# Kernel tuning notes

Hardware: AMD Instinct MI355X
Metric: run time of the kernel (lower is better)

The kernel has to match this reference:

```python
import jax, jax.numpy as jnp
import numpy as np

N, E, P = 50000, 800000, 100000
IN, HID, K = 128, 128, 2


def _tagconv(h, nw, src, dst, n, W, b, k=K):
    # DGL TAGConv with edge_weight: k edge-weighted SpMM hops, concat, linear.
    feats = [h]
    for _ in range(k):
        m = feats[-1][src] * nw[:, None]          # [E, d] gather-multiply
        feats.append(jax.ops.segment_sum(m, dst, num_segments=n))
    return jnp.concatenate(feats, axis=-1) @ W.T + b


def setup_inputs() -> dict:
    key = jax.random.key(0)
    ks = jax.random.split(key, 24)
    inp = {
        "x": jax.random.normal(ks[0], (N, IN), jnp.float32),
        "w": jax.random.uniform(ks[1], (E,), jnp.float32, 0.01, 1.0),
        "src": jax.random.randint(ks[2], (E,), 0, N),
        "dst": jax.random.randint(ks[3], (E,), 0, N),
        "pos_src": jax.random.randint(ks[4], (P,), 0, N),
        "pos_dst": jax.random.randint(ks[5], (P,), 0, N),
        "neg_src": jax.random.randint(ks[6], (P,), 0, N),
        "neg_dst": jax.random.randint(ks[7], (P,), 0, N),
        # TAGConv linear weights: [hid, (k+1)*d_in]
        "W0": jax.random.normal(ks[8], (HID, (K + 1) * IN), jnp.float32) * 0.05,
        "b0": jnp.zeros((HID,), jnp.float32),
        "W1": jax.random.normal(ks[9], (HID, (K + 1) * HID), jnp.float32) * 0.05,
        "b1": jnp.zeros((HID,), jnp.float32),
        "W2": jax.random.normal(ks[10], (HID, (K + 1) * HID), jnp.float32) * 0.05,
        "b2": jnp.zeros((HID,), jnp.float32),
        # predictor MLP
        "Wp1": jax.random.normal(ks[11], (HID, HID), jnp.float32) * 0.05,
        "bp1": jnp.zeros((HID,), jnp.float32),
        "Wp2": jax.random.normal(ks[12], (HID, HID), jnp.float32) * 0.05,
        "bp2": jnp.zeros((HID,), jnp.float32),
        "Wp3": jax.random.normal(ks[13], (1, HID), jnp.float32) * 0.05,
        "bp3": jnp.zeros((1,), jnp.float32),
    }
    return inp


def reference(x, w, src, dst, pos_src, pos_dst, neg_src, neg_dst,
              W0, b0, W1, b1, W2, b2, Wp1, bp1, Wp2, bp2, Wp3, bp3):
    n = x.shape[0]
    # EdgeWeightNorm('both'): w_e / sqrt(deg_out_w(src) * deg_in_w(dst))
    deg_out = jax.ops.segment_sum(w, src, num_segments=n)
    deg_in = jax.ops.segment_sum(w, dst, num_segments=n)
    denom = jnp.sqrt(jnp.clip(deg_out[src] * deg_in[dst], 1e-12))
    nw = w / denom

    h = _tagconv(x, nw, src, dst, n, W0, b0)
    h = jax.nn.relu(h)
    h = _tagconv(h, nw, src, dst, n, W1, b1)
    h = jax.nn.relu(h)
    h = _tagconv(h, nw, src, dst, n, W2, b2)

    def predictor(z):
        z = jax.nn.relu(z @ Wp1.T + bp1)
        z = jax.nn.relu(z @ Wp2.T + bp2)
        return z @ Wp3.T + bp3

    h_pos = predictor(h[pos_src] * h[pos_dst])
    h_neg = predictor(h[neg_src] * h[neg_dst])
    return h_pos, h_neg, h
```

## Files before the change

### kernel.cpp

```cpp
#include <hip/hip_runtime.h>
#include <stdint.h>


#define D128 128

typedef __bf16 v8bf __attribute__((ext_vector_type(8)));
typedef float v4f __attribute__((ext_vector_type(4)));
typedef uint32_t v4u __attribute__((ext_vector_type(4)));
typedef unsigned short ushort_t;

union BFU { v4u u; v8bf b; uint4 q; };

__device__ __forceinline__ uint32_t pack_hl(float f) {
  uint32_t hi = __float_as_uint(f) & 0xffff0000u;
  float lo = f - __uint_as_float(hi);
  return hi | (__float_as_uint(lo) >> 16);
}
__device__ __forceinline__ float unpack_hl(uint32_t p) {
  return __uint_as_float(p & 0xffff0000u) + __uint_as_float(p << 16);
}
__device__ __forceinline__ uint32_t f2bf_rn(float f) {
  uint32_t u = __float_as_uint(f);
  return (u + 0x7fffu + ((u >> 16) & 1u)) >> 16;
}
// ... 130 lines not shown
#pragma unroll
    for (int k = 0; k < 4; ++k) { uint32_t tmp = ws4[k]; ws4[k] = a; a += tmp; }
  }
  __syncthreads();
  uint32_t ex = x - v + ws4[wid];
  cur[t] = ex;
  int d = hb * 256 + t;
  if (d < N) rowptr[d] = b + (int)ex;
  __syncthreads();
  for (int i = b + t; i < e; i += 256) {
    uint2 el = bufD[i];
    uint32_t lo = (el.x >> 16) & 255u;
    uint32_t pos = atomicAdd(&cur[lo], 1u);
    esw[b + pos] = make_uint2(el.x & 0xffffu, el.y);
  }
}

__global__ void k_sub_src(const uint2* __restrict__ bufS,
                          const uint32_t* __restrict__ baseS,
                          float* __restrict__ deg_out, int N) {
  __shared__ float acc[256];
  int hb = blockIdx.x, t = threadIdx.x;
  acc[t] = 0.f;
  __syncthreads();
  int b = (int)baseS[hb], e = (int)baseS[hb + 1];
  for (int i = b + t; i < e; i += 256)
    atomicAdd(&acc[bufS[i].x & 255u], __uint_as_float(bufS[i].y));
  __syncthreads();
  int s = hb * 256 + t;
  if (s < N) deg_out[s] = acc[t];
}

__global__ void k_norm(const float* __restrict__ deg_out, const int* __restrict__ rowptr,
                       uint2* __restrict__ esw, int n) {
  int row = blockIdx.x * 4 + (threadIdx.x >> 6);
  if (row >= n) return;
  int lane = threadIdx.x & 63;
  int b0 = rowptr[row];
  int cnt = rowptr[row + 1] - b0;
  if (cnt <= 64) {
    uint32_t key = 0xffffffffu;
    float val = 0.f;
    if (lane < cnt) {
      uint2 e = esw[b0 + lane];
      key = e.x;
      val = __uint_as_float(e.y);
    }
    float s = val;
#pragma unroll
    for (int d = 32; d; d >>= 1) s += __shfl_xor(s, d);
#pragma unroll
    for (int k = 2; k <= 64; k <<= 1) {
#pragma unroll
      for (int j = k >> 1; j > 0; j >>= 1) {
        uint32_t ok = (uint32_t)__shfl_xor((int)key, j);
        float ov = __shfl_xor(val, j);
        bool asc = ((lane & k) == 0);
        bool lower = ((lane & j) == 0);
        bool take_min = (lower == asc);
        bool sw = take_min ? (ok < key) : (ok > key);
        if (sw) { key = ok; val = ov; }
      }
    }
    if (lane < cnt) {
      float dout = deg_out[key];
      float nw = val / sqrtf(fmaxf(dout * s, 1e-12f));
      esw[b0 + lane] = make_uint2(key, __float_as_uint(nw));
    }
  } else {
    float s = 0.f;
    for (int i = lane; i < cnt; i += 64) s += __uint_as_float(esw[b0 + i].y);
#pragma unroll
    for (int d = 32; d; d >>= 1) s += __shfl_xor(s, d);
    for (int i = lane; i < cnt; i += 64) {
      uint2 e = esw[b0 + i];
      float dout = deg_out[e.x];
      float nw = __uint_as_float(e.y) / sqrtf(fmaxf(dout * s, 1e-12f));
      esw[b0 + i] = make_uint2(e.x, __float_as_uint(nw));
    }
  }
}


__global__ void k_pack4(const float* __restrict__ in, uint32_t* __restrict__ Xp,
                        uint32_t* __restrict__ Xb, int n4) {
  int i = blockIdx.x * 256 + threadIdx.x;
  if (i >= n4) return;
  float4 f = ((const float4*)in)[i];
  ((uint4*)Xp)[i] = make_uint4(pack_hl(f.x), pack_hl(f.y), pack_hl(f.z), pack_hl(f.w));
  uint2 b;
  b.x = f2bf_rn(f.x) | (f2bf_rn(f.y) << 16);
  b.y = f2bf_rn(f.z) | (f2bf_rn(f.w) << 16);
  ((uint2*)Xb)[i] = b;
}

__global__ void k_packW(const float* __restrict__ p0, const float* __restrict__ p1,
                        const float* __restrict__ p2, const float* __restrict__ p3,
                        const float* __restrict__ p4, ushort_t* __restrict__ out) {
  int i = blockIdx.x * 256 + threadIdx.x;
  if (i >= 180224) return;
  float f;
  if (i < 49152) f = p0[i];
  else if (i < 98304) f = p1[i - 49152];
  else if (i < 147456) f = p2[i - 98304];
  else if (i < 163840) f = p3[i - 147456];
  else f = p4[i - 163840];
  out[i] = (ushort_t)f2bf_rn(f);
}


__global__ void k_spmm(const uint32_t* __restrict__ X, uint32_t* __restrict__ Y,
                       const uint2* __restrict__ esw, const int* __restrict__ rowptr,
                       int n) {
  int row = blockIdx.x * 4 + (threadIdx.x >> 6);
  if (row >= n) return;
  int lane = threadIdx.x & 63;
  int b0 = rowptr[row];
  int cnt = rowptr[row + 1] - b0;
  const uint32_t* __restrict__ Xl = X + lane;
  float a0 = 0.f, a1 = 0.f, c0 = 0.f, c1 = 0.f;
  for (int cbase = 0; cbase < cnt; cbase += 64) {
    int cc = min(64, cnt - cbase);
    int srcv = 0, wbits = 0;
    if (lane < cc) {
      uint2 e = esw[(size_t)b0 + cbase + lane];
      srcv = (int)e.x;
      wbits = (int)e.y;
    }
    int i = 0;
    for (; i + 8 <= cc; i += 8) {
      uint32_t u[8];
      float wv[8];
#pragma unroll
      for (int j = 0; j < 8; ++j) {
        int sj = __builtin_amdgcn_readlane(srcv, i + j);
        wv[j] = __uint_as_float(__builtin_amdgcn_readlane(wbits, i + j));
        u[j] = Xl[(size_t)sj * 64];
      }
#pragma unroll
      for (int j = 0; j < 8; j += 2) {
        a0 = fmaf(wv[j], bflo(u[j]), a0);
        a1 = fmaf(wv[j], bfhi(u[j]), a1);
        c0 = fmaf(wv[j + 1], bflo(u[j + 1]), c0);
        c1 = fmaf(wv[j + 1], bfhi(u[j + 1]), c1);
      }
    }
    for (; i < cc; ++i) {
      int sj = __builtin_amdgcn_readlane(srcv, i);
      float w0 = __uint_as_float(__builtin_amdgcn_readlane(wbits, i));
      uint32_t u0 = Xl[(size_t)sj * 64];
      a0 = fmaf(w0, bflo(u0), a0);
      a1 = fmaf(w0, bfhi(u0), a1);
    }
  }
  Y[(size_t)row * 64 + lane] = f2bf_rn(a0 + c0) | (f2bf_rn(a1 + c1) << 16);
}


__device__ __forceinline__ void build_frags(const uint32_t* __restrict__ p,
                                            v8bf& hi, v8bf& lo) {
  uint4 q0 = *(const uint4*)p;
  uint4 q1 = *(const uint4*)(p + 4);
  BFU uh, ul;
  uh.u[0] = (q0.x >> 16) | (q0.y & 0xffff0000u);
  uh.u[1] = (q0.z >> 16) | (q0.w & 0xffff0000u);
  uh.u[2] = (q1.x >> 16) | (q1.y & 0xffff0000u);
  uh.u[3] = (q1.z >> 16) | (q1.w & 0xffff0000u);
  ul.u[0] = (q0.x & 0xffffu) | (q0.y << 16);
  ul.u[1] = (q0.z & 0xffffu) | (q0.w << 16);
  ul.u[2] = (q1.x & 0xffffu) | (q1.y << 16);
  ul.u[3] = (q1.z & 0xffffu) | (q1.w << 16);
  hi = uh.b;
  lo = ul.b;
}

__global__ __launch_bounds__(256) void k_gemm(
    const uint32_t* __restrict__ F0hl, const uint32_t* __restrict__ F1b,
    const uint32_t* __restrict__ F2b, const ushort_t* __restrict__ Wb,
    const float* __restrict__ bias, int relu, int M,
    uint32_t* __restrict__ outp, ushort_t* __restrict__ outh,
    float* __restrict__ outf) {
  __shared__ ushort_t Wl[128 * 128];
  const int t = threadIdx.x;
  const int lane = t & 63;
  const int wave = t >> 6;
  const int wr = wave >> 1, wc = wave & 1;
  const int row0 = blockIdx.x * 64;
  const int l15 = lane & 15;
  const int kg = lane >> 4;

  int arow[2];
#pragma unroll
  for (int mr = 0; mr < 2; ++mr)
    arow[mr] = min(row0 + wr * 32 + mr * 16 + l15, M - 1);
  int wcol[4];
  float bv[4];
#pragma unroll
  for (int nr = 0; nr < 4; ++nr) {
    wcol[nr] = wc * 64 + nr * 16 + l15;
    bv[nr] = bias[wcol[nr]];
  }

  v4f acc[2][4];
#pragma unroll
  for (int mr = 0; mr < 2; ++mr)
#pragma unroll
    for (int nr = 0; nr < 4; ++nr) acc[mr][nr] = (v4f){0.f, 0.f, 0.f, 0.f};

  const int sc = t >> 1;
  const int sh = t & 1;

  for (int seg = 0; seg < 3; ++seg) {
    __syncthreads();
    {
      const ushort_t* gp = Wb + (size_t)sc * 384 + seg * 128 + sh * 64;
#pragma unroll
      for (int gi = 0; gi < 8; ++gi) {
        int gg = sh * 8 + gi;
        uint4 v = *(const uint4*)(gp + gi * 8);
        *(uint4*)((char*)Wl + sc * 256 + ((gg ^ (sc & 7)) * 16)) = v;
      }
    }
    __syncthreads();
    for (int kc = 0; kc < 128; kc += 32) {
      const int ko = kc + kg * 8;
      if (seg == 0) {
        v8bf ah[2], al[2];
#pragma unroll
        for (int mr = 0; mr < 2; ++mr)
          build_frags(F0hl + (size_t)arow[mr] * D128 + ko, ah[mr], al[mr]);
#pragma unroll
        for (int nr = 0; nr < 4; ++nr) {
          int col = wcol[nr];
          int g = (kc >> 3) + kg;
          v8bf bf = *(const v8bf*)((const char*)Wl + col * 256 + ((g ^ (col & 7)) * 16));
#pragma unroll
          for (int mr = 0; mr < 2; ++mr) {
            acc[mr][nr] = __builtin_amdgcn_mfma_f32_16x16x32_bf16(ah[mr], bf, acc[mr][nr], 0, 0, 0);
            acc[mr][nr] = __builtin_amdgcn_mfma_f32_16x16x32_bf16(al[mr], bf, acc[mr][nr], 0, 0, 0);
          }
        }
      } else {
        const uint32_t* __restrict__ Fb = (seg == 1) ? F1b : F2b;
        v8bf af[2];
#pragma unroll
        for (int mr = 0; mr < 2; ++mr) {
          BFU u;
          u.q = *(const uint4*)(Fb + (size_t)arow[mr] * 64 + (kc >> 1) + kg * 4);
          af[mr] = u.b;
        }
#pragma unroll
        for (int nr = 0; nr < 4; ++nr) {
          int col = wcol[nr];
          int g = (kc >> 3) + kg;
          v8bf bf = *(const v8bf*)((const char*)Wl + col * 256 + ((g ^ (col & 7)) * 16));
#pragma unroll
          for (int mr = 0; mr < 2; ++mr)
            acc[mr][nr] = __builtin_amdgcn_mfma_f32_16x16x32_bf16(af[mr], bf, acc[mr][nr], 0, 0, 0);
        }
      }
    }
  }

  __syncthreads();

#pragma unroll
  for (int mr = 0; mr < 2; ++mr) {
#pragma unroll
    for (int nr = 0; nr < 4; ++nr) {
      v4f a = acc[mr][nr];
#pragma unroll
      for (int r = 0; r < 4; ++r) {
        int row = row0 + wr * 32 + mr * 16 + kg * 4 + r;
        if (row < M) {
          float v = a[r] + bv[nr];
          if (relu) v = fmaxf(v, 0.f);
          size_t o = (size_t)row * D128 + wcol[nr];
          if (outp) outp[o] = pack_hl(v);
          if (outh) outh[o] = (ushort_t)f2bf_rn(v);
          if (outf) outf[o] = v;
        }
      }
    }
  }
}


__global__ __launch_bounds__(256) void k_pred(
    const uint32_t* __restrict__ Hb, const int* __restrict__ pos_src,
    const int* __restrict__ pos_dst, const int* __restrict__ neg_src,
    const int* __restrict__ neg_dst, const ushort_t* __restrict__ W1,
    const ushort_t* __restrict__ W2, const float* __restrict__ b1,
    const float* __restrict__ b2, const float* __restrict__ w3,
    const float* __restrict__ b3, int P, float* __restrict__ out) {
  __shared__ ushort_t Wl[128 * 128];
  const int t = threadIdx.x;
  const int lane = t & 63;
  const int wave = t >> 6;
  const int l15 = lane & 15;
  const int kg = lane >> 4;
  const int q = blockIdx.x * 64 + wave * 16 + l15;
  const int P2 = 2 * P;
  const bool valid = q < P2;
  const int qc = valid ? q : (P2 - 1);
  const int ia = (qc < P) ? pos_src[qc] : neg_src[qc - P];
  const int ib = (qc < P) ? pos_dst[qc] : neg_dst[qc - P];

  const int sc = t >> 1;
  const int sh = t & 1;

  {
    const ushort_t* gp = W1 + sc * 128 + sh * 64;
#pragma unroll
    for (int gi = 0; gi < 8; ++gi) {
      int gg = sh * 8 + gi;
      uint4 v = *(const uint4*)(gp + gi * 8);
      *(uint4*)((char*)Wl + sc * 256 + ((gg ^ (sc & 7)) * 16)) = v;
    }
  }

  v8bf zf[4];
#pragma unroll
  for (int kc = 0; kc < 4; ++kc) {
    uint4 qa = *(const uint4*)(Hb + (size_t)ia * 64 + kc * 16 + kg * 4);
    uint4 qb = *(const uint4*)(Hb + (size_t)ib * 64 + kc * 16 + kg * 4);
    BFU z;
    z.u[0] = bfmul2(qa.x, qb.x);
    z.u[1] = bfmul2(qa.y, qb.y);
    z.u[2] = bfmul2(qa.z, qb.z);
    z.u[3] = bfmul2(qa.w, qb.w);
    zf[kc] = z.b;
  }
  __syncthreads();

  v4f acc1[8];
#pragma unroll
  for (int nr = 0; nr < 8; ++nr) acc1[nr] = (v4f){0.f, 0.f, 0.f, 0.f};
#pragma unroll
  for (int kc = 0; kc < 4; ++kc) {
#pragma unroll
    for (int nr = 0; nr < 8; ++nr) {
      int c = nr * 16 + l15;
      int g = 4 * kc + kg;
      v8bf wf = *(const v8bf*)((const char*)Wl + c * 256 + ((g ^ (c & 7)) * 16));
      acc1[nr] = __builtin_amdgcn_mfma_f32_16x16x32_bf16(wf, zf[kc], acc1[nr], 0, 0, 0);
    }
  }

  uint32_t pk[8][2];
#pragma unroll
  for (int nr = 0; nr < 8; ++nr) {
    float v[4];
#pragma unroll
    for (int r = 0; r < 4; ++r) {
      int c = nr * 16 + kg * 4 + r;
      v[r] = fmaxf(acc1[nr][r] + b1[c], 0.f);
    }
    pk[nr][0] = f2bf_rn(v[0]) | (f2bf_rn(v[1]) << 16);
    pk[nr][1] = f2bf_rn(v[2]) | (f2bf_rn(v[3]) << 16);
  }

  __syncthreads();
  {
    const ushort_t* gp = W2 + sc * 128 + sh * 64;
#pragma unroll
    for (int gi = 0; gi < 8; ++gi) {
      int gg = sh * 8 + gi;
      uint4 v = *(const uint4*)(gp + gi * 8);
      *(uint4*)((char*)Wl + sc * 256 + ((gg ^ (sc & 7)) * 16)) = v;
    }
  }
  __syncthreads();

  v4f acc2[8];
#pragma unroll
  for (int nr = 0; nr < 8; ++nr) acc2[nr] = (v4f){0.f, 0.f, 0.f, 0.f};
#pragma unroll
  for (int kc = 0; kc < 4; ++kc) {
    BFU y;
#pragma unroll
    for (int d = 0; d < 4; ++d) {
      int srcLane = l15 + 16 * ((kg & 1) * 2 + (d >> 1));
      int va = __shfl((int)pk[2 * kc][d & 1], srcLane);
      int vb = __shfl((int)pk[2 * kc + 1][d & 1], srcLane);
      y.u[d] = (kg & 2) ? (uint32_t)vb : (uint32_t)va;
    }
#pragma unroll
    for (int nr = 0; nr < 8; ++nr) {
      int c = nr * 16 + l15;
      int g = 4 * kc + kg;
      v8bf wf = *(const v8bf*)((const char*)Wl + c * 256 + ((g ^ (c & 7)) * 16));
      acc2[nr] = __builtin_amdgcn_mfma_f32_16x16x32_bf16(wf, y.b, acc2[nr], 0, 0, 0);
    }
  }

  float s = 0.f;
#pragma unroll
  for (int nr = 0; nr < 8; ++nr) {
#pragma unroll
    for (int r = 0; r < 4; ++r) {
      int c = nr * 16 + kg * 4 + r;
      s += fmaxf(acc2[nr][r] + b2[c], 0.f) * w3[c];
    }
  }
  s += __shfl_xor(s, 16);
  s += __shfl_xor(s, 32);
  if (valid && kg == 0) out[q] = s + b3[0];
}


extern "C" void kernel_launch(void* const* d_in, const int* in_sizes, int n_in,
                              void* d_out, int out_size, void* d_ws, size_t ws_size,
                              hipStream_t stream) {
  const float* x = (const float*)d_in[0];
  const float* w = (const float*)d_in[1];
  const int* src = (const int*)d_in[2];
  const int* dst = (const int*)d_in[3];
  const int* pos_src = (const int*)d_in[4];
  const int* pos_dst = (const int*)d_in[5];
  const int* neg_src = (const int*)d_in[6];
  const int* neg_dst = (const int*)d_in[7];
  const float* W0 = (const float*)d_in[8];
  const float* b0 = (const float*)d_in[9];
  const float* W1 = (const float*)d_in[10];
  const float* b1 = (const float*)d_in[11];
  const float* W2 = (const float*)d_in[12];
  const float* b2 = (const float*)d_in[13];
  const float* Wp1 = (const float*)d_in[14];
  const float* bp1 = (const float*)d_in[15];
  const float* Wp2 = (const float*)d_in[16];
  const float* bp2 = (const float*)d_in[17];
  const float* Wp3 = (const float*)d_in[18];
  const float* bp3 = (const float*)d_in[19];

  const int N = in_sizes[0] / D128;
  const int E = in_sizes[1];
  const int P = in_sizes[4];

  float* out = (float*)d_out;
  float* h_fin = out + 2 * (size_t)P;
  uint32_t* Hp = (uint32_t*)h_fin;

  char* p = (char*)d_ws;
#define WALLOC(T, name, bytes) \
  T name = (T)p;               \
  p += (((size_t)(bytes) + 255) & ~(size_t)255);
  WALLOC(uint32_t*, meta, (size_t)(4 * 256 + 2 * 257) * 4)
  WALLOC(float*, deg_out, (size_t)N * 4)
  WALLOC(int*, rowptr, (size_t)(N + 1) * 4)
  WALLOC(uint2*, bufD, (size_t)E * 8)
  WALLOC(uint2*, bufS, (size_t)E * 8)
  WALLOC(uint2*, esw, (size_t)E * 8)
  WALLOC(ushort_t*, Wpk, (size_t)180224 * 2)
  WALLOC(uint32_t*, Xp, (size_t)N * D128 * 4)
  WALLOC(uint32_t*, Xb, (size_t)N * 64 * 4)
  WALLOC(uint32_t*, A, (size_t)N * 64 * 4)
  WALLOC(uint32_t*, B, (size_t)N * 64 * 4)
  WALLOC(uint32_t*, Hbuf, (size_t)N * 64 * 4)
#undef WALLOC

  uint32_t* histD = meta;
  uint32_t* histS = meta + 256;
  uint32_t* curD = meta + 512;
  uint32_t* curS = meta + 768;
  uint32_t* baseD = meta + 1024;
  uint32_t* baseS = meta + 1024 + 257;

  const ushort_t* W0b = Wpk;
  const ushort_t* W1b = Wpk + 49152;
  const ushort_t* W2b = Wpk + 98304;
  const ushort_t* Wp1b = Wpk + 147456;
  const ushort_t* Wp2b = Wpk + 163840;

  const int rb = (N + 3) / 4;
  const int gg = (N + 63) / 64;
  const int nHi = (N + 255) >> 8;

  hipMemsetAsync(meta, 0, 4 * 256 * 4, stream);
  k_hist2<<<128, 256, 0, stream>>>(src, dst, E, histD, histS);
  k_scan2<<<1, 256, 0, stream>>>(histD, histS, curD, baseD, curS, baseS, rowptr, N, E);
  k_part_dst<<<128, 256, 0, stream>>>(src, dst, w, E, curD, bufD);
  k_part_src<<<128, 256, 0, stream>>>(src, w, E, curS, bufS);
  k_sub_dst<<<nHi, 256, 0, stream>>>(bufD, baseD, esw, rowptr, N);
  k_sub_src<<<nHi, 256, 0, stream>>>(bufS, baseS, deg_out, N);
  k_norm<<<rb, 256, 0, stream>>>(deg_out, rowptr, esw, N);

  k_pack4<<<(N * 32 + 255) / 256, 256, 0, stream>>>(x, Xp, Xb, N * 32);
  k_packW<<<(180224 + 255) / 256, 256, 0, stream>>>(W0, W1, W2, Wp1, Wp2, Wpk);

  k_spmm<<<rb, 256, 0, stream>>>(Xb, A, esw, rowptr, N);
  k_spmm<<<rb, 256, 0, stream>>>(A, B, esw, rowptr, N);
  k_gemm<<<gg, 256, 0, stream>>>(Xp, A, B, W0b, b0, 1, N, Hp, (ushort_t*)Hbuf, nullptr);
  k_spmm<<<rb, 256, 0, stream>>>(Hbuf, A, esw, rowptr, N);
  k_spmm<<<rb, 256, 0, stream>>>(A, B, esw, rowptr, N);
  k_gemm<<<gg, 256, 0, stream>>>(Hp, A, B, W1b, b1, 1, N, Xp, (ushort_t*)Hbuf, nullptr);
  k_spmm<<<rb, 256, 0, stream>>>(Hbuf, A, esw, rowptr, N);
  k_spmm<<<rb, 256, 0, stream>>>(A, B, esw, rowptr, N);
  k_gemm<<<gg, 256, 0, stream>>>(Xp, A, B, W2b, b2, 0, N, nullptr, (ushort_t*)B, h_fin);

  k_pred<<<(2 * P + 63) / 64, 256, 0, stream>>>(B, pos_src, pos_dst, neg_src, neg_dst,
                                                Wp1b, Wp2b, bp1, bp2, Wp3, bp3, P, out);
}
```

Before: 454.0 us.

## Half-wave SpMM rows, prefetched GEMM operands, and src-sorted predictor queries

The SpMM now assigns two rows per wave, each 32-lane half loading 8 bytes per neighbor, which halves the wave count and widens loads. The GEMM prefetches A-operand fragments into registers before the weight-staging barrier so global latency overlaps LDS staging. Predictor queries are bucket-sorted by source node through three new small kernels, so gathered rows have better cache locality. The cost is extra launches and register pressure, plus divergence when the two rows in a wave have very different degrees.

```diff
diff --git a/kernel.cpp b/kernel.cpp
--- a/kernel.cpp
+++ b/kernel.cpp
@@ -236,6 +236,71 @@
 }
 
 
+__global__ void k_phist(const int* __restrict__ pos_src, const int* __restrict__ neg_src,
+                        int P, uint32_t* __restrict__ ph) {
+  __shared__ uint32_t h[256];
+  int t = threadIdx.x;
+  h[t] = 0;
+  __syncthreads();
+  int P2 = 2 * P;
+  for (int iq = blockIdx.x * 256 + t; iq < P2; iq += gridDim.x * 256) {
+    int ia = (iq < P) ? pos_src[iq] : neg_src[iq - P];
+    atomicAdd(&h[((unsigned)ia) >> 8], 1u);
+  }
+  __syncthreads();
+  if (h[t]) atomicAdd(&ph[t], h[t]);
+}
+
+__global__ void k_pscan(const uint32_t* __restrict__ ph, uint32_t* __restrict__ pcur) {
+  __shared__ uint32_t ws4[4];
+  int t = threadIdx.x;
+  int lane = t & 63, wid = t >> 6;
+  uint32_t v = ph[t], x = v;
+#pragma unroll
+  for (int d = 1; d < 64; d <<= 1) {
+    uint32_t y = (uint32_t)__shfl_up((int)x, d);
+    if (lane >= d) x += y;
+  }
+  if (lane == 63) ws4[wid] = x;
+  __syncthreads();
+  if (t == 0) {
+    uint32_t a = 0;
+#pragma unroll
+    for (int k = 0; k < 4; ++k) { uint32_t tmp = ws4[k]; ws4[k] = a; a += tmp; }
+  }
+  __syncthreads();
+  pcur[t] = x - v + ws4[wid];
+}
+
+__global__ void k_ppart(const int* __restrict__ pos_src, const int* __restrict__ neg_src,
+                        int P, uint32_t* __restrict__ pcur,
+                        uint32_t* __restrict__ qsorted) {
+  __shared__ uint32_t lh[256], lbase[256];
+  int t = threadIdx.x;
+  int P2 = 2 * P;
+  int per = (P2 + gridDim.x - 1) / gridDim.x;
+  int e0 = blockIdx.x * per, e1 = min(e0 + per, P2);
+  lh[t] = 0;
+  __syncthreads();
+  for (int iq = e0 + t; iq < e1; iq += 256) {
+    int ia = (iq < P) ? pos_src[iq] : neg_src[iq - P];
+    atomicAdd(&lh[((unsigned)ia) >> 8], 1u);
+  }
+  __syncthreads();
+  uint32_t c = lh[t];
+  lbase[t] = c ? atomicAdd(&pcur[t], c) : 0u;
+  __syncthreads();
+  lh[t] = 0;
+  __syncthreads();
+  for (int iq = e0 + t; iq < e1; iq += 256) {
+    int ia = (iq < P) ? pos_src[iq] : neg_src[iq - P];
+    uint32_t bin = ((unsigned)ia) >> 8;
+    uint32_t pos = lbase[bin] + atomicAdd(&lh[bin], 1u);
+    qsorted[pos] = (uint32_t)iq;
+  }
+}
+
+
 __global__ void k_pack4(const float* __restrict__ in, uint32_t* __restrict__ Xp,
                         uint32_t* __restrict__ Xb, int n4) {
   int i = blockIdx.x * 256 + threadIdx.x;
@@ -266,55 +331,70 @@
 __global__ void k_spmm(const uint32_t* __restrict__ X, uint32_t* __restrict__ Y,
                        const uint2* __restrict__ esw, const int* __restrict__ rowptr,
                        int n) {
-  int row = blockIdx.x * 4 + (threadIdx.x >> 6);
-  if (row >= n) return;
-  int lane = threadIdx.x & 63;
-  int b0 = rowptr[row];
-  int cnt = rowptr[row + 1] - b0;
-  const uint32_t* __restrict__ Xl = X + lane;
-  float a0 = 0.f, a1 = 0.f, c0 = 0.f, c1 = 0.f;
-  for (int cbase = 0; cbase < cnt; cbase += 64) {
-    int cc = min(64, cnt - cbase);
-    int srcv = 0, wbits = 0;
-    if (lane < cc) {
-      uint2 e = esw[(size_t)b0 + cbase + lane];
+  int rowbase = blockIdx.x * 8 + ((threadIdx.x >> 6) << 1);
+  int half = (threadIdx.x >> 5) & 1;
+  int l32 = threadIdx.x & 31;
+  int row = rowbase + half;
+  bool valid = row < n;
+  int rowc = valid ? row : (n - 1);
+  int b0 = rowptr[rowc];
+  int cnt = valid ? (rowptr[rowc + 1] - b0) : 0;
+  int hbase = half << 5;
+
+  const uint32_t* __restrict__ Xl = X + 2 * l32;
+  float a0 = 0.f, a1 = 0.f, a2 = 0.f, a3 = 0.f;
+
+  int cntO = __shfl(cnt, hbase ^ 32);
+  int cntM = max(cnt, cntO);
+
+  for (int cbase = 0; cbase < cntM; cbase += 32) {
+    int cc = min(max(cnt - cbase, 0), 32);
+    int srcv = 0; uint32_t wbits = 0;
+    if (l32 < cc) {
+      uint2 e = esw[(size_t)b0 + cbase + l32];
       srcv = (int)e.x;
-      wbits = (int)e.y;
-    }
+      wbits = e.y;
+    }
+    int ccO = __shfl(cc, hbase ^ 32);
+    int ccM = max(cc, ccO);
     int i = 0;
-    for (; i + 8 <= cc; i += 8) {
-      uint32_t u[8];
+    for (; i + 8 <= ccM; i += 8) {
+      uint2 u[8];
       float wv[8];
 #pragma unroll
       for (int j = 0; j < 8; ++j) {
-        int sj = __builtin_amdgcn_readlane(srcv, i + j);
-        wv[j] = __uint_as_float(__builtin_amdgcn_readlane(wbits, i + j));
-        u[j] = Xl[(size_t)sj * 64];
+        int s = __shfl(srcv, hbase + i + j);
+        wv[j] = __uint_as_float((uint32_t)__shfl((int)wbits, hbase + i + j));
+        u[j] = *(const uint2*)(Xl + (size_t)s * 64);
       }
 #pragma unroll
-      for (int j = 0; j < 8; j += 2) {
-        a0 = fmaf(wv[j], bflo(u[j]), a0);
-        a1 = fmaf(wv[j], bfhi(u[j]), a1);
-        c0 = fmaf(wv[j + 1], bflo(u[j + 1]), c0);
-        c1 = fmaf(wv[j + 1], bfhi(u[j + 1]), c1);
+      for (int j = 0; j < 8; ++j) {
+        a0 = fmaf(wv[j], bflo(u[j].x), a0);
+        a1 = fmaf(wv[j], bfhi(u[j].x), a1);
+        a2 = fmaf(wv[j], bflo(u[j].y), a2);
+        a3 = fmaf(wv[j], bfhi(u[j].y), a3);
       }
     }
-    for (; i < cc; ++i) {
-      int sj = __builtin_amdgcn_readlane(srcv, i);
-      float w0 = __uint_as_float(__builtin_amdgcn_readlane(wbits, i));
-      uint32_t u0 = Xl[(size_t)sj * 64];
-      a0 = fmaf(w0, bflo(u0), a0);
-      a1 = fmaf(w0, bfhi(u0), a1);
-    }
-  }
-  Y[(size_t)row * 64 + lane] = f2bf_rn(a0 + c0) | (f2bf_rn(a1 + c1) << 16);
-}
-
-
-__device__ __forceinline__ void build_frags(const uint32_t* __restrict__ p,
-                                            v8bf& hi, v8bf& lo) {
-  uint4 q0 = *(const uint4*)p;
-  uint4 q1 = *(const uint4*)(p + 4);
+    for (; i < ccM; ++i) {
+      int s = __shfl(srcv, hbase + i);
+      float wv = __uint_as_float((uint32_t)__shfl((int)wbits, hbase + i));
+      uint2 u = *(const uint2*)(Xl + (size_t)s * 64);
+      a0 = fmaf(wv, bflo(u.x), a0);
+      a1 = fmaf(wv, bfhi(u.x), a1);
+      a2 = fmaf(wv, bflo(u.y), a2);
+      a3 = fmaf(wv, bfhi(u.y), a3);
+    }
+  }
+  if (valid) {
+    uint2 o;
+    o.x = f2bf_rn(a0) | (f2bf_rn(a1) << 16);
+    o.y = f2bf_rn(a2) | (f2bf_rn(a3) << 16);
+    *(uint2*)(Y + (size_t)row * 64 + 2 * l32) = o;
+  }
+}
+
+
+__device__ __forceinline__ void build_frags_v(uint4 q0, uint4 q1, v8bf& hi, v8bf& lo) {
   BFU uh, ul;
   uh.u[0] = (q0.x >> 16) | (q0.y & 0xffff0000u);
   uh.u[1] = (q0.z >> 16) | (q0.w & 0xffff0000u);
@@ -355,6 +435,13 @@
     bv[nr] = bias[wcol[nr]];
   }
 
+  const uint32_t* __restrict__ F0r0 = F0hl + (size_t)arow[0] * D128 + kg * 8;
+  const uint32_t* __restrict__ F0r1 = F0hl + (size_t)arow[1] * D128 + kg * 8;
+  const uint32_t* __restrict__ F1r0 = F1b + (size_t)arow[0] * 64 + kg * 4;
+  const uint32_t* __restrict__ F1r1 = F1b + (size_t)arow[1] * 64 + kg * 4;
+  const uint32_t* __restrict__ F2r0 = F2b + (size_t)arow[0] * 64 + kg * 4;
+  const uint32_t* __restrict__ F2r1 = F2b + (size_t)arow[1] * 64 + kg * 4;
+
   v4f acc[2][4];
 #pragma unroll
   for (int mr = 0; mr < 2; ++mr)
@@ -363,55 +450,92 @@
 
   const int sc = t >> 1;
   const int sh = t & 1;
-
-  for (int seg = 0; seg < 3; ++seg) {
+  const ushort_t* gpW = Wb + (size_t)sc * 384 + sh * 64;
+  char* WlBase = (char*)Wl + sc * 256;
+
+  uint4 f0[4][2][2];
+#pragma unroll
+  for (int kc = 0; kc < 2; ++kc) {
+    f0[kc][0][0] = *(const uint4*)(F0r0 + kc * 32);
+    f0[kc][0][1] = *(const uint4*)(F0r0 + kc * 32 + 4);
+    f0[kc][1][0] = *(const uint4*)(F0r1 + kc * 32);
+    f0[kc][1][1] = *(const uint4*)(F0r1 + kc * 32 + 4);
+  }
+  __syncthreads();
+  {
+    const ushort_t* gp = gpW;
+#pragma unroll
+    for (int gi = 0; gi < 8; ++gi) {
+      int gg = sh * 8 + gi;
+      uint4 v = *(const uint4*)(gp + gi * 8);
+      *(uint4*)(WlBase + ((gg ^ (sc & 7)) * 16)) = v;
+    }
+  }
+  __syncthreads();
+#pragma unroll
+  for (int kc = 0; kc < 4; ++kc) {
+    if (kc < 2) {
+      f0[kc + 2][0][0] = *(const uint4*)(F0r0 + (kc + 2) * 32);
+      f0[kc + 2][0][1] = *(const uint4*)(F0r0 + (kc + 2) * 32 + 4);
+      f0[kc + 2][1][0] = *(const uint4*)(F0r1 + (kc + 2) * 32);
+      f0[kc + 2][1][1] = *(const uint4*)(F0r1 + (kc + 2) * 32 + 4);
+    }
+    v8bf ah[2], al[2];
+#pragma unroll
+    for (int mr = 0; mr < 2; ++mr)
+      build_frags_v(f0[kc][mr][0], f0[kc][mr][1], ah[mr], al[mr]);
+#pragma unroll
+    for (int nr = 0; nr < 4; ++nr) {
+      int col = wcol[nr];
+      int g = (kc << 2) + kg;
+      v8bf bf = *(const v8bf*)((const char*)Wl + col * 256 + ((g ^ (col & 7)) * 16));
+#pragma unroll
+      for (int mr = 0; mr < 2; ++mr) {
+        acc[mr][nr] = __builtin_amdgcn_mfma_f32_16x16x32_bf16(ah[mr], bf, acc[mr][nr], 0, 0, 0);
+        acc[mr][nr] = __builtin_amdgcn_mfma_f32_16x16x32_bf16(al[mr], bf, acc[mr][nr], 0, 0, 0);
+      }
+    }
+  }
+
+#pragma unroll
+  for (int seg = 1; seg < 3; ++seg) {
+    const uint32_t* __restrict__ Fr0 = (seg == 1) ? F1r0 : F2r0;
+    const uint32_t* __restrict__ Fr1 = (seg == 1) ? F1r1 : F2r1;
+    uint4 fb[4][2];
+#pragma unroll
+    for (int kc = 0; kc < 4; ++kc) {
+      fb[kc][0] = *(const uint4*)(Fr0 + kc * 16);
+      fb[kc][1] = *(const uint4*)(Fr1 + kc * 16);
+    }
     __syncthreads();
     {
-      const ushort_t* gp = Wb + (size_t)sc * 384 + seg * 128 + sh * 64;
+      const ushort_t* gp = gpW + seg * 128;
 #pragma unroll
       for (int gi = 0; gi < 8; ++gi) {
         int gg = sh * 8 + gi;
         uint4 v = *(const uint4*)(gp + gi * 8);
-        *(uint4*)((char*)Wl + sc * 256 + ((gg ^ (sc & 7)) * 16)) = v;
+        *(uint4*)(WlBase + ((gg ^ (sc & 7)) * 16)) = v;
       }
     }
     __syncthreads();
-    for (int kc = 0; kc < 128; kc += 32) {
-      const int ko = kc + kg * 8;
-      if (seg == 0) {
-        v8bf ah[2], al[2];
+#pragma unroll
+    for (int kc = 0; kc < 4; ++kc) {
+      v8bf af[2];
+      {
+        BFU u0, u1;
+        u0.q = fb[kc][0];
+        u1.q = fb[kc][1];
+        af[0] = u0.b;
+        af[1] = u1.b;
+      }
+#pragma unroll
+      for (int nr = 0; nr < 4; ++nr) {
+        int col = wcol[nr];
+        int g = (kc << 2) + kg;
+        v8bf bf = *(const v8bf*)((const char*)Wl + col * 256 + ((g ^ (col & 7)) * 16));
 #pragma unroll
         for (int mr = 0; mr < 2; ++mr)
-          build_frags(F0hl + (size_t)arow[mr] * D128 + ko, ah[mr], al[mr]);
-#pragma unroll
-        for (int nr = 0; nr < 4; ++nr) {
-          int col = wcol[nr];
-          int g = (kc >> 3) + kg;
-          v8bf bf = *(const v8bf*)((const char*)Wl + col * 256 + ((g ^ (col & 7)) * 16));
-#pragma unroll
-          for (int mr = 0; mr < 2; ++mr) {
-            acc[mr][nr] = __builtin_amdgcn_mfma_f32_16x16x32_bf16(ah[mr], bf, acc[mr][nr], 0, 0, 0);
-            acc[mr][nr] = __builtin_amdgcn_mfma_f32_16x16x32_bf16(al[mr], bf, acc[mr][nr], 0, 0, 0);
-          }
-        }
-      } else {
-        const uint32_t* __restrict__ Fb = (seg == 1) ? F1b : F2b;
-        v8bf af[2];
-#pragma unroll
-        for (int mr = 0; mr < 2; ++mr) {
-          BFU u;
-          u.q = *(const uint4*)(Fb + (size_t)arow[mr] * 64 + (kc >> 1) + kg * 4);
-          af[mr] = u.b;
-        }
-#pragma unroll
-        for (int nr = 0; nr < 4; ++nr) {
-          int col = wcol[nr];
-          int g = (kc >> 3) + kg;
-          v8bf bf = *(const v8bf*)((const char*)Wl + col * 256 + ((g ^ (col & 7)) * 16));
-#pragma unroll
-          for (int mr = 0; mr < 2; ++mr)
-            acc[mr][nr] = __builtin_amdgcn_mfma_f32_16x16x32_bf16(af[mr], bf, acc[mr][nr], 0, 0, 0);
-        }
+          acc[mr][nr] = __builtin_amdgcn_mfma_f32_16x16x32_bf16(af[mr], bf, acc[mr][nr], 0, 0, 0);
       }
     }
   }
@@ -441,24 +565,25 @@
 
 
 __global__ __launch_bounds__(256) void k_pred(
-    const uint32_t* __restrict__ Hb, const int* __restrict__ pos_src,
-    const int* __restrict__ pos_dst, const int* __restrict__ neg_src,
-    const int* __restrict__ neg_dst, const ushort_t* __restrict__ W1,
-    const ushort_t* __restrict__ W2, const float* __restrict__ b1,
-    const float* __restrict__ b2, const float* __restrict__ w3,
-    const float* __restrict__ b3, int P, float* __restrict__ out) {
+    const uint32_t* __restrict__ Hb, const uint32_t* __restrict__ qsorted,
+    const int* __restrict__ pos_src, const int* __restrict__ pos_dst,
+    const int* __restrict__ neg_src, const int* __restrict__ neg_dst,
+    const ushort_t* __restrict__ W1, const ushort_t* __restrict__ W2,
+    const float* __restrict__ b1, const float* __restrict__ b2,
+    const float* __restrict__ w3, const float* __restrict__ b3, int P,
+    float* __restrict__ out) {
   __shared__ ushort_t Wl[128 * 128];
   const int t = threadIdx.x;
   const int lane = t & 63;
   const int wave = t >> 6;
   const int l15 = lane & 15;
   const int kg = lane >> 4;
-  const int q = blockIdx.x * 64 + wave * 16 + l15;
+  const int idx = blockIdx.x * 64 + wave * 16 + l15;
   const int P2 = 2 * P;
-  const bool valid = q < P2;
-  const int qc = valid ? q : (P2 - 1);
-  const int ia = (qc < P) ? pos_src[qc] : neg_src[qc - P];
-  const int ib = (qc < P) ? pos_dst[qc] : neg_dst[qc - P];
+  const bool valid = idx < P2;
+  const int iq = valid ? (int)qsorted[idx] : (P2 - 1);
+  const int ia = (iq < P) ? pos_src[iq] : neg_src[iq - P];
+  const int ib = (iq < P) ? pos_dst[iq] : neg_dst[iq - P];
 
   const int sc = t >> 1;
   const int sh = t & 1;
@@ -559,7 +684,7 @@
   }
   s += __shfl_xor(s, 16);
   s += __shfl_xor(s, 32);
-  if (valid && kg == 0) out[q] = s + b3[0];
+  if (valid && kg == 0) out[iq] = s + b3[0];
 }
 
 
@@ -600,8 +725,10 @@
   T name = (T)p;               \
   p += (((size_t)(bytes) + 255) & ~(size_t)255);
   WALLOC(uint32_t*, meta, (size_t)(4 * 256 + 2 * 257) * 4)
+  WALLOC(uint32_t*, pmeta, (size_t)512 * 4)
   WALLOC(float*, deg_out, (size_t)N * 4)
   WALLOC(int*, rowptr, (size_t)(N + 1) * 4)
+  WALLOC(uint32_t*, qsorted, (size_t)2 * P * 4)
   WALLOC(uint2*, bufD, (size_t)E * 8)
   WALLOC(uint2*, bufS, (size_t)E * 8)
   WALLOC(uint2*, esw, (size_t)E * 8)
@@ -619,6 +746,8 @@
   uint32_t* curS = meta + 768;
   uint32_t* baseD = meta + 1024;
   uint32_t* baseS = meta + 1024 + 257;
+  uint32_t* ph = pmeta;
+  uint32_t* pcur = pmeta + 256;
 
   const ushort_t* W0b = Wpk;
   const ushort_t* W1b = Wpk + 49152;
@@ -627,10 +756,12 @@
   const ushort_t* Wp2b = Wpk + 163840;
 
   const int rb = (N + 3) / 4;
+  const int rb2 = (N + 7) / 8;
   const int gg = (N + 63) / 64;
   const int nHi = (N + 255) >> 8;
 
   hipMemsetAsync(meta, 0, 4 * 256 * 4, stream);
+  hipMemsetAsync(ph, 0, 256 * 4, stream);
   k_hist2<<<128, 256, 0, stream>>>(src, dst, E, histD, histS);
   k_scan2<<<1, 256, 0, stream>>>(histD, histS, curD, baseD, curS, baseS, rowptr, N, E);
   k_part_dst<<<128, 256, 0, stream>>>(src, dst, w, E, curD, bufD);
@@ -639,19 +770,24 @@
   k_sub_src<<<nHi, 256, 0, stream>>>(bufS, baseS, deg_out, N);
   k_norm<<<rb, 256, 0, stream>>>(deg_out, rowptr, esw, N);
 
+  k_phist<<<64, 256, 0, stream>>>(pos_src, neg_src, P, ph);
+  k_pscan<<<1, 256, 0, stream>>>(ph, pcur);
+  k_ppart<<<64, 256, 0, stream>>>(pos_src, neg_src, P, pcur, qsorted);
+
   k_pack4<<<(N * 32 + 255) / 256, 256, 0, stream>>>(x, Xp, Xb, N * 32);
   k_packW<<<(180224 + 255) / 256, 256, 0, stream>>>(W0, W1, W2, Wp1, Wp2, Wpk);
 
-  k_spmm<<<rb, 256, 0, stream>>>(Xb, A, esw, rowptr, N);
-  k_spmm<<<rb, 256, 0, stream>>>(A, B, esw, rowptr, N);
+  k_spmm<<<rb2, 256, 0, stream>>>(Xb, A, esw, rowptr, N);
+  k_spmm<<<rb2, 256, 0, stream>>>(A, B, esw, rowptr, N);
   k_gemm<<<gg, 256, 0, stream>>>(Xp, A, B, W0b, b0, 1, N, Hp, (ushort_t*)Hbuf, nullptr);
-  k_spmm<<<rb, 256, 0, stream>>>(Hbuf, A, esw, rowptr, N);
-  k_spmm<<<rb, 256, 0, stream>>>(A, B, esw, rowptr, N);
+  k_spmm<<<rb2, 256, 0, stream>>>(Hbuf, A, esw, rowptr, N);
+  k_spmm<<<rb2, 256, 0, stream>>>(A, B, esw, rowptr, N);
   k_gemm<<<gg, 256, 0, stream>>>(Hp, A, B, W1b, b1, 1, N, Xp, (ushort_t*)Hbuf, nullptr);
-  k_spmm<<<rb, 256, 0, stream>>>(Hbuf, A, esw, rowptr, N);
-  k_spmm<<<rb, 256, 0, stream>>>(A, B, esw, rowptr, N);
+  k_spmm<<<rb2, 256, 0, stream>>>(Hbuf, A, esw, rowptr, N);
+  k_spmm<<<rb2, 256, 0, stream>>>(A, B, esw, rowptr, N);
   k_gemm<<<gg, 256, 0, stream>>>(Xp, A, B, W2b, b2, 0, N, nullptr, (ushort_t*)B, h_fin);
 
-  k_pred<<<(2 * P + 63) / 64, 256, 0, stream>>>(B, pos_src, pos_dst, neg_src, neg_dst,
-                                                Wp1b, Wp2b, bp1, bp2, Wp3, bp3, P, out);
-}
+  k_pred<<<(2 * P + 63) / 64, 256, 0, stream>>>(B, qsorted, pos_src, pos_dst, neg_src,
+                                                neg_dst, Wp1b, Wp2b, bp1, bp2, Wp3, bp3,
+                                                P, out);
+}
```

Measured after the change: 466.4 us. 2.7% more time.

## Prefetch GEMM operands, uniform-load SpMM edges, and double predictor work per block

Applied to the files above, without the earlier changes.

The SpMM kernel now makes the row index wave-uniform and loads edge (src, weight) pairs directly per edge instead of staging them through lanes with readlane. The GEMM kernel preloads A-operand fragments into registers before the weight staging barrier and unrolls the segment loop so global loads overlap LDS fills. The predictor kernel handles two query groups per block, which halves how often the weights are staged into shared memory and issues more gathers in flight. These changes trade higher register pressure, and possibly lower occupancy, for more memory-level parallelism and fewer redundant weight loads.

```diff
diff --git a/kernel.cpp b/kernel.cpp
--- a/kernel.cpp
+++ b/kernel.cpp
@@ -268,53 +268,42 @@
                        int n) {
   int row = blockIdx.x * 4 + (threadIdx.x >> 6);
   if (row >= n) return;
+  row = __builtin_amdgcn_readfirstlane(row);
   int lane = threadIdx.x & 63;
   int b0 = rowptr[row];
   int cnt = rowptr[row + 1] - b0;
-  const uint32_t* __restrict__ Xl = X + lane;
+  const uint2* __restrict__ ep = esw + b0;
   float a0 = 0.f, a1 = 0.f, c0 = 0.f, c1 = 0.f;
-  for (int cbase = 0; cbase < cnt; cbase += 64) {
-    int cc = min(64, cnt - cbase);
-    int srcv = 0, wbits = 0;
-    if (lane < cc) {
-      uint2 e = esw[(size_t)b0 + cbase + lane];
-      srcv = (int)e.x;
-      wbits = (int)e.y;
-    }
-    int i = 0;
-    for (; i + 8 <= cc; i += 8) {
-      uint32_t u[8];
-      float wv[8];
-#pragma unroll
-      for (int j = 0; j < 8; ++j) {
-        int sj = __builtin_amdgcn_readlane(srcv, i + j);
-        wv[j] = __uint_as_float(__builtin_amdgcn_readlane(wbits, i + j));
-        u[j] = Xl[(size_t)sj * 64];
-      }
-#pragma unroll
-      for (int j = 0; j < 8; j += 2) {
-        a0 = fmaf(wv[j], bflo(u[j]), a0);
-        a1 = fmaf(wv[j], bfhi(u[j]), a1);
-        c0 = fmaf(wv[j + 1], bflo(u[j + 1]), c0);
-        c1 = fmaf(wv[j + 1], bfhi(u[j + 1]), c1);
-      }
-    }
-    for (; i < cc; ++i) {
-      int sj = __builtin_amdgcn_readlane(srcv, i);
-      float w0 = __uint_as_float(__builtin_amdgcn_readlane(wbits, i));
-      uint32_t u0 = Xl[(size_t)sj * 64];
-      a0 = fmaf(w0, bflo(u0), a0);
-      a1 = fmaf(w0, bfhi(u0), a1);
-    }
+  int i = 0;
+  for (; i + 8 <= cnt; i += 8) {
+    uint2 e[8];
+#pragma unroll
+    for (int j = 0; j < 8; ++j) e[j] = ep[i + j];
+    uint32_t u[8];
+#pragma unroll
+    for (int j = 0; j < 8; ++j) u[j] = *(X + (size_t)e[j].x * 64 + lane);
+#pragma unroll
+    for (int j = 0; j < 8; j += 2) {
+      float w0 = __uint_as_float(e[j].y);
+      float w1 = __uint_as_float(e[j + 1].y);
+      a0 = fmaf(w0, bflo(u[j]), a0);
+      a1 = fmaf(w0, bfhi(u[j]), a1);
+      c0 = fmaf(w1, bflo(u[j + 1]), c0);
+      c1 = fmaf(w1, bfhi(u[j + 1]), c1);
+    }
+  }
+  for (; i < cnt; ++i) {
+    uint2 e = ep[i];
+    uint32_t u = *(X + (size_t)e.x * 64 + lane);
+    float w0 = __uint_as_float(e.y);
+    a0 = fmaf(w0, bflo(u), a0);
+    a1 = fmaf(w0, bfhi(u), a1);
   }
   Y[(size_t)row * 64 + lane] = f2bf_rn(a0 + c0) | (f2bf_rn(a1 + c1) << 16);
 }
 
 
-__device__ __forceinline__ void build_frags(const uint32_t* __restrict__ p,
-                                            v8bf& hi, v8bf& lo) {
-  uint4 q0 = *(const uint4*)p;
-  uint4 q1 = *(const uint4*)(p + 4);
+__device__ __forceinline__ void build_frags_v(uint4 q0, uint4 q1, v8bf& hi, v8bf& lo) {
   BFU uh, ul;
   uh.u[0] = (q0.x >> 16) | (q0.y & 0xffff0000u);
   uh.u[1] = (q0.z >> 16) | (q0.w & 0xffff0000u);
@@ -355,6 +344,13 @@
     bv[nr] = bias[wcol[nr]];
   }
 
+  const uint32_t* __restrict__ F0r0 = F0hl + (size_t)arow[0] * D128 + kg * 8;
+  const uint32_t* __restrict__ F0r1 = F0hl + (size_t)arow[1] * D128 + kg * 8;
+  const uint32_t* __restrict__ F1r0 = F1b + (size_t)arow[0] * 64 + kg * 4;
+  const uint32_t* __restrict__ F1r1 = F1b + (size_t)arow[1] * 64 + kg * 4;
+  const uint32_t* __restrict__ F2r0 = F2b + (size_t)arow[0] * 64 + kg * 4;
+  const uint32_t* __restrict__ F2r1 = F2b + (size_t)arow[1] * 64 + kg * 4;
+
   v4f acc[2][4];
 #pragma unroll
   for (int mr = 0; mr < 2; ++mr)
@@ -363,55 +359,92 @@
 
   const int sc = t >> 1;
   const int sh = t & 1;
-
-  for (int seg = 0; seg < 3; ++seg) {
+  const ushort_t* gpW = Wb + (size_t)sc * 384 + sh * 64;
+  char* WlBase = (char*)Wl + sc * 256;
+
+  uint4 f0[4][2][2];
+#pragma unroll
+  for (int kc = 0; kc < 2; ++kc) {
+    f0[kc][0][0] = *(const uint4*)(F0r0 + kc * 32);
+    f0[kc][0][1] = *(const uint4*)(F0r0 + kc * 32 + 4);
+    f0[kc][1][0] = *(const uint4*)(F0r1 + kc * 32);
+    f0[kc][1][1] = *(const uint4*)(F0r1 + kc * 32 + 4);
+  }
+  __syncthreads();
+  {
+    const ushort_t* gp = gpW;
+#pragma unroll
+    for (int gi = 0; gi < 8; ++gi) {
+      int gg = sh * 8 + gi;
+      uint4 v = *(const uint4*)(gp + gi * 8);
+      *(uint4*)(WlBase + ((gg ^ (sc & 7)) * 16)) = v;
+    }
+  }
+  __syncthreads();
+#pragma unroll
+  for (int kc = 0; kc < 4; ++kc) {
+    if (kc < 2) {
+      f0[kc + 2][0][0] = *(const uint4*)(F0r0 + (kc + 2) * 32);
+      f0[kc + 2][0][1] = *(const uint4*)(F0r0 + (kc + 2) * 32 + 4);
+      f0[kc + 2][1][0] = *(const uint4*)(F0r1 + (kc + 2) * 32);
+      f0[kc + 2][1][1] = *(const uint4*)(F0r1 + (kc + 2) * 32 + 4);
+    }
+    v8bf ah[2], al[2];
+#pragma unroll
+    for (int mr = 0; mr < 2; ++mr)
+      build_frags_v(f0[kc][mr][0], f0[kc][mr][1], ah[mr], al[mr]);
+#pragma unroll
+    for (int nr = 0; nr < 4; ++nr) {
+      int col = wcol[nr];
+      int g = (kc << 2) + kg;
+      v8bf bf = *(const v8bf*)((const char*)Wl + col * 256 + ((g ^ (col & 7)) * 16));
+#pragma unroll
+      for (int mr = 0; mr < 2; ++mr) {
+        acc[mr][nr] = __builtin_amdgcn_mfma_f32_16x16x32_bf16(ah[mr], bf, acc[mr][nr], 0, 0, 0);
+        acc[mr][nr] = __builtin_amdgcn_mfma_f32_16x16x32_bf16(al[mr], bf, acc[mr][nr], 0, 0, 0);
+      }
+    }
+  }
+
+#pragma unroll
+  for (int seg = 1; seg < 3; ++seg) {
+    const uint32_t* __restrict__ Fr0 = (seg == 1) ? F1r0 : F2r0;
+    const uint32_t* __restrict__ Fr1 = (seg == 1) ? F1r1 : F2r1;
+    uint4 fb[4][2];
+#pragma unroll
+    for (int kc = 0; kc < 4; ++kc) {
+      fb[kc][0] = *(const uint4*)(Fr0 + kc * 16);
+      fb[kc][1] = *(const uint4*)(Fr1 + kc * 16);
+    }
     __syncthreads();
     {
-      const ushort_t* gp = Wb + (size_t)sc * 384 + seg * 128 + sh * 64;
+      const ushort_t* gp = gpW + seg * 128;
 #pragma unroll
       for (int gi = 0; gi < 8; ++gi) {
         int gg = sh * 8 + gi;
         uint4 v = *(const uint4*)(gp + gi * 8);
-        *(uint4*)((char*)Wl + sc * 256 + ((gg ^ (sc & 7)) * 16)) = v;
+        *(uint4*)(WlBase + ((gg ^ (sc & 7)) * 16)) = v;
       }
     }
     __syncthreads();
-    for (int kc = 0; kc < 128; kc += 32) {
-      const int ko = kc + kg * 8;
-      if (seg == 0) {
-        v8bf ah[2], al[2];
+#pragma unroll
+    for (int kc = 0; kc < 4; ++kc) {
+      v8bf af[2];
+      {
+        BFU u0, u1;
+        u0.q = fb[kc][0];
+        u1.q = fb[kc][1];
+        af[0] = u0.b;
+        af[1] = u1.b;
+      }
+#pragma unroll
+      for (int nr = 0; nr < 4; ++nr) {
+        int col = wcol[nr];
+        int g = (kc << 2) + kg;
+        v8bf bf = *(const v8bf*)((const char*)Wl + col * 256 + ((g ^ (col & 7)) * 16));
 #pragma unroll
         for (int mr = 0; mr < 2; ++mr)
-          build_frags(F0hl + (size_t)arow[mr] * D128 + ko, ah[mr], al[mr]);
-#pragma unroll
-        for (int nr = 0; nr < 4; ++nr) {
-          int col = wcol[nr];
-          int g = (kc >> 3) + kg;
-          v8bf bf = *(const v8bf*)((const char*)Wl + col * 256 + ((g ^ (col & 7)) * 16));
-#pragma unroll
-          for (int mr = 0; mr < 2; ++mr) {
-            acc[mr][nr] = __builtin_amdgcn_mfma_f32_16x16x32_bf16(ah[mr], bf, acc[mr][nr], 0, 0, 0);
-            acc[mr][nr] = __builtin_amdgcn_mfma_f32_16x16x32_bf16(al[mr], bf, acc[mr][nr], 0, 0, 0);
-          }
-        }
-      } else {
-        const uint32_t* __restrict__ Fb = (seg == 1) ? F1b : F2b;
-        v8bf af[2];
-#pragma unroll
-        for (int mr = 0; mr < 2; ++mr) {
-          BFU u;
-          u.q = *(const uint4*)(Fb + (size_t)arow[mr] * 64 + (kc >> 1) + kg * 4);
-          af[mr] = u.b;
-        }
-#pragma unroll
-        for (int nr = 0; nr < 4; ++nr) {
-          int col = wcol[nr];
-          int g = (kc >> 3) + kg;
-          v8bf bf = *(const v8bf*)((const char*)Wl + col * 256 + ((g ^ (col & 7)) * 16));
-#pragma unroll
-          for (int mr = 0; mr < 2; ++mr)
-            acc[mr][nr] = __builtin_amdgcn_mfma_f32_16x16x32_bf16(af[mr], bf, acc[mr][nr], 0, 0, 0);
-        }
+          acc[mr][nr] = __builtin_amdgcn_mfma_f32_16x16x32_bf16(af[mr], bf, acc[mr][nr], 0, 0, 0);
       }
     }
   }
@@ -453,12 +486,17 @@
   const int wave = t >> 6;
   const int l15 = lane & 15;
   const int kg = lane >> 4;
-  const int q = blockIdx.x * 64 + wave * 16 + l15;
   const int P2 = 2 * P;
-  const bool valid = q < P2;
-  const int qc = valid ? q : (P2 - 1);
-  const int ia = (qc < P) ? pos_src[qc] : neg_src[qc - P];
-  const int ib = (qc < P) ? pos_dst[qc] : neg_dst[qc - P];
+
+  const int qA = blockIdx.x * 128 + wave * 16 + l15;
+  const int qB = qA + 64;
+  const bool vA = qA < P2, vB = qB < P2;
+  const int qcA = vA ? qA : (P2 - 1);
+  const int qcB = vB ? qB : (P2 - 1);
+  const int iaA = (qcA < P) ? pos_src[qcA] : neg_src[qcA - P];
+  const int ibA = (qcA < P) ? pos_dst[qcA] : neg_dst[qcA - P];
+  const int iaB = (qcB < P) ? pos_src[qcB] : neg_src[qcB - P];
+  const int ibB = (qcB < P) ? pos_dst[qcB] : neg_dst[qcB - P];
 
   const int sc = t >> 1;
   const int sh = t & 1;
@@ -473,45 +511,79 @@
     }
   }
 
-  v8bf zf[4];
+  uint4 gaA[4], gbA[4], gaB[4], gbB[4];
 #pragma unroll
   for (int kc = 0; kc < 4; ++kc) {
-    uint4 qa = *(const uint4*)(Hb + (size_t)ia * 64 + kc * 16 + kg * 4);
-    uint4 qb = *(const uint4*)(Hb + (size_t)ib * 64 + kc * 16 + kg * 4);
-    BFU z;
-    z.u[0] = bfmul2(qa.x, qb.x);
-    z.u[1] = bfmul2(qa.y, qb.y);
-    z.u[2] = bfmul2(qa.z, qb.z);
-    z.u[3] = bfmul2(qa.w, qb.w);
-    zf[kc] = z.b;
-  }
-  __syncthreads();
-
-  v4f acc1[8];
-#pragma unroll
-  for (int nr = 0; nr < 8; ++nr) acc1[nr] = (v4f){0.f, 0.f, 0.f, 0.f};
+    gaA[kc] = *(const uint4*)(Hb + (size_t)iaA * 64 + kc * 16 + kg * 4);
+    gbA[kc] = *(const uint4*)(Hb + (size_t)ibA * 64 + kc * 16 + kg * 4);
+    gaB[kc] = *(const uint4*)(Hb + (size_t)iaB * 64 + kc * 16 + kg * 4);
+    gbB[kc] = *(const uint4*)(Hb + (size_t)ibB * 64 + kc * 16 + kg * 4);
+  }
+  v8bf zfA[4], zfB[4];
 #pragma unroll
   for (int kc = 0; kc < 4; ++kc) {
+    BFU zA, zB;
+    zA.u[0] = bfmul2(gaA[kc].x, gbA[kc].x);
+    zA.u[1] = bfmul2(gaA[kc].y, gbA[kc].y);
+    zA.u[2] = bfmul2(gaA[kc].z, gbA[kc].z);
+    zA.u[3] = bfmul2(gaA[kc].w, gbA[kc].w);
+    zB.u[0] = bfmul2(gaB[kc].x, gbB[kc].x);
+    zB.u[1] = bfmul2(gaB[kc].y, gbB[kc].y);
+    zB.u[2] = bfmul2(gaB[kc].z, gbB[kc].z);
+    zB.u[3] = bfmul2(gaB[kc].w, gbB[kc].w);
+    zfA[kc] = zA.b;
+    zfB[kc] = zB.b;
+  }
+  __syncthreads();
+
+  uint32_t pkA[8][2], pkB[8][2];
+  {
+    v4f acc1[8];
+#pragma unroll
+    for (int nr = 0; nr < 8; ++nr) acc1[nr] = (v4f){0.f, 0.f, 0.f, 0.f};
+#pragma unroll
+    for (int kc = 0; kc < 4; ++kc) {
+#pragma unroll
+      for (int nr = 0; nr < 8; ++nr) {
+        int c = nr * 16 + l15;
+        int g = 4 * kc + kg;
+        v8bf wf = *(const v8bf*)((const char*)Wl + c * 256 + ((g ^ (c & 7)) * 16));
+        acc1[nr] = __builtin_amdgcn_mfma_f32_16x16x32_bf16(wf, zfA[kc], acc1[nr], 0, 0, 0);
+      }
+    }
 #pragma unroll
     for (int nr = 0; nr < 8; ++nr) {
-      int c = nr * 16 + l15;
-      int g = 4 * kc + kg;
-      v8bf wf = *(const v8bf*)((const char*)Wl + c * 256 + ((g ^ (c & 7)) * 16));
-      acc1[nr] = __builtin_amdgcn_mfma_f32_16x16x32_bf16(wf, zf[kc], acc1[nr], 0, 0, 0);
-    }
-  }
-
-  uint32_t pk[8][2];
-#pragma unroll
-  for (int nr = 0; nr < 8; ++nr) {
-    float v[4];
-#pragma unroll
-    for (int r = 0; r < 4; ++r) {
-      int c = nr * 16 + kg * 4 + r;
-      v[r] = fmaxf(acc1[nr][r] + b1[c], 0.f);
-    }
-    pk[nr][0] = f2bf_rn(v[0]) | (f2bf_rn(v[1]) << 16);
-    pk[nr][1] = f2bf_rn(v[2]) | (f2bf_rn(v[3]) << 16);
+      float v0 = fmaxf(acc1[nr][0] + b1[nr * 16 + kg * 4 + 0], 0.f);
+      float v1 = fmaxf(acc1[nr][1] + b1[nr * 16 + kg * 4 + 1], 0.f);
+      float v2 = fmaxf(acc1[nr][2] + b1[nr * 16 + kg * 4 + 2], 0.f);
+      float v3 = fmaxf(acc1[nr][3] + b1[nr * 16 + kg * 4 + 3], 0.f);
+      pkA[nr][0] = f2bf_rn(v0) | (f2bf_rn(v1) << 16);
+      pkA[nr][1] = f2bf_rn(v2) | (f2bf_rn(v3) << 16);
+    }
+  }
+  {
+    v4f acc1[8];
+#pragma unroll
+    for (int nr = 0; nr < 8; ++nr) acc1[nr] = (v4f){0.f, 0.f, 0.f, 0.f};
+#pragma unroll
+    for (int kc = 0; kc < 4; ++kc) {
+#pragma unroll
+      for (int nr = 0; nr < 8; ++nr) {
+        int c = nr * 16 + l15;
+        int g = 4 * kc + kg;
+        v8bf wf = *(const v8bf*)((const char*)Wl + c * 256 + ((g ^ (c & 7)) * 16));
+        acc1[nr] = __builtin_amdgcn_mfma_f32_16x16x32_bf16(wf, zfB[kc], acc1[nr], 0, 0, 0);
+      }
+    }
+#pragma unroll
+    for (int nr = 0; nr < 8; ++nr) {
+      float v0 = fmaxf(acc1[nr][0] + b1[nr * 16 + kg * 4 + 0], 0.f);
+      float v1 = fmaxf(acc1[nr][1] + b1[nr * 16 + kg * 4 + 1], 0.f);
+      float v2 = fmaxf(acc1[nr][2] + b1[nr * 16 + kg * 4 + 2], 0.f);
+      float v3 = fmaxf(acc1[nr][3] + b1[nr * 16 + kg * 4 + 3], 0.f);
+      pkB[nr][0] = f2bf_rn(v0) | (f2bf_rn(v1) << 16);
+      pkB[nr][1] = f2bf_rn(v2) | (f2bf_rn(v3) << 16);
+    }
   }
 
   __syncthreads();
@@ -526,40 +598,52 @@
   }
   __syncthreads();
 
-  v4f acc2[8];
-#pragma unroll
-  for (int nr = 0; nr < 8; ++nr) acc2[nr] = (v4f){0.f, 0.f, 0.f, 0.f};
-#pragma unroll
-  for (int kc = 0; kc < 4; ++kc) {
-    BFU y;
-#pragma unroll
-    for (int d = 0; d < 4; ++d) {
-      int srcLane = l15 + 16 * ((kg & 1) * 2 + (d >> 1));
-      int va = __shfl((int)pk[2 * kc][d & 1], srcLane);
-      int vb = __shfl((int)pk[2 * kc + 1][d & 1], srcLane);
-      y.u[d] = (kg & 2) ? (uint32_t)vb : (uint32_t)va;
-    }
+#pragma unroll
+  for (int chunk = 0; chunk < 2; ++chunk) {
+    v4f acc2[8];
+#pragma unroll
+    for (int nr = 0; nr < 8; ++nr) acc2[nr] = (v4f){0.f, 0.f, 0.f, 0.f};
+#pragma unroll
+    for (int kc = 0; kc < 4; ++kc) {
+      BFU y;
+#pragma unroll
+      for (int d = 0; d < 4; ++d) {
+        int srcLane = l15 + 16 * ((kg & 1) * 2 + (d >> 1));
+        uint32_t w0, w1;
+        if (chunk == 0) {
+          w0 = (uint32_t)__shfl((int)pkA[2 * kc][d & 1], srcLane);
+          w1 = (uint32_t)__shfl((int)pkA[2 * kc + 1][d & 1], srcLane);
+        } else {
+          w0 = (uint32_t)__shfl((int)pkB[2 * kc][d & 1], srcLane);
+          w1 = (uint32_t)__shfl((int)pkB[2 * kc + 1][d & 1], srcLane);
+        }
+        y.u[d] = (kg & 2) ? w1 : w0;
+      }
+#pragma unroll
+      for (int nr = 0; nr < 8; ++nr) {
+        int c = nr * 16 + l15;
+        int g = 4 * kc + kg;
+        v8bf wf = *(const v8bf*)((const char*)Wl + c * 256 + ((g ^ (c & 7)) * 16));
+        acc2[nr] = __builtin_amdgcn_mfma_f32_16x16x32_bf16(wf, y.b, acc2[nr], 0, 0, 0);
+      }
+    }
+    float s = 0.f;
 #pragma unroll
     for (int nr = 0; nr < 8; ++nr) {
-      int c = nr * 16 + l15;
-      int g = 4 * kc + kg;
-      v8bf wf = *(const v8bf*)((const char*)Wl + c * 256 + ((g ^ (c & 7)) * 16));
-      acc2[nr] = __builtin_amdgcn_mfma_f32_16x16x32_bf16(wf, y.b, acc2[nr], 0, 0, 0);
-    }
-  }
-
-  float s = 0.f;
-#pragma unroll
-  for (int nr = 0; nr < 8; ++nr) {
-#pragma unroll
-    for (int r = 0; r < 4; ++r) {
-      int c = nr * 16 + kg * 4 + r;
-      s += fmaxf(acc2[nr][r] + b2[c], 0.f) * w3[c];
-    }
-  }
-  s += __shfl_xor(s, 16);
-  s += __shfl_xor(s, 32);
-  if (valid && kg == 0) out[q] = s + b3[0];
+#pragma unroll
+      for (int r = 0; r < 4; ++r) {
+        int c = nr * 16 + kg * 4 + r;
+        s += fmaxf(acc2[nr][r] + b2[c], 0.f) * w3[c];
+      }
+    }
+    s += __shfl_xor(s, 16);
+    s += __shfl_xor(s, 32);
+    if (chunk == 0) {
+      if (vA && kg == 0) out[qA] = s + b3[0];
+    } else {
+      if (vB && kg == 0) out[qB] = s + b3[0];
+    }
+  }
 }
 
 
@@ -652,6 +736,6 @@
   k_spmm<<<rb, 256, 0, stream>>>(A, B, esw, rowptr, N);
   k_gemm<<<gg, 256, 0, stream>>>(Xp, A, B, W2b, b2, 0, N, nullptr, (ushort_t*)B, h_fin);
 
-  k_pred<<<(2 * P + 63) / 64, 256, 0, stream>>>(B, pos_src, pos_dst, neg_src, neg_dst,
-                                                Wp1b, Wp2b, bp1, bp2, Wp3, bp3, P, out);
-}
+  k_pred<<<(2 * P + 127) / 128, 256, 0, stream>>>(B, pos_src, pos_dst, neg_src, neg_dst,
+                                                  Wp1b, Wp2b, bp1, bp2, Wp3, bp3, P, out);
+}
```

Result: no change. 445.7 us (-1.8%).
